# Kernel tuning notes

Hardware: AMD Instinct MI355X
Metric: run time of the kernel (lower is better)

Reference implementation:

```python
import jax, jax.numpy as jnp
from jax import lax
import numpy as np

NEG_SLOPE = 0.01  # torch leaky_relu default
KSIZE = 5

def lrelu(x):
    return jax.nn.leaky_relu(x, NEG_SLOPE)

def conv(x, w, b):
    # x: [N,C,H,W], w: [O,I,kh,kw], valid padding (pad=False in ConvChain)
    y = lax.conv_general_dilated(x, w, (1, 1), 'VALID',
                                 dimension_numbers=('NCHW', 'OIHW', 'NCHW'))
    return y + b[None, :, None, None]

def _forward(features, radiance, global_features,
             emb_w0, emb_b0, emb_w, emb_b,
             pf_w0, pf_b0, pf_w1, pf_b1, pf_w2, pf_b2,
             sf_w, sf_b,
             kp_w0, kp_b0, kp_w1, kp_b1, kp_w2, kp_b2):
    bs, spp, nf, h, w = features.shape
    ngf = global_features.shape[1]
    K = KSIZE

    # --- sample_embedding over all samples at once (replaces per-sp loop) ---
    g = jnp.broadcast_to(global_features, (bs, ngf, h, w))
    x = jnp.concatenate(
        [jnp.broadcast_to(g[:, None], (bs, spp, ngf, h, w)), features], axis=2)
    x = x.reshape(bs * spp, ngf + nf, h, w)
    x = lrelu(conv(x, emb_w0, emb_b0))
    for i in range(5):  # hidden conv layers 1..5
        x = lrelu(conv(x, emb_w[i], emb_b[i]))
    x = conv(x, emb_w[5], emb_b[5])  # linear output layer
    pixel_embed = x.reshape(bs, spp, x.shape[1], x.shape[2], x.shape[3]).max(axis=1)

    # --- pixel_features chain (3 layers, last linear) ---
    p = lrelu(conv(pixel_embed, pf_w0, pf_b0))
    p = lrelu(conv(p, pf_w1, pf_b1))
    pfeat = conv(p, pf_w2, pf_b2)  # [bs, pair_width, ph, pw]
    ph, pw = pfeat.shape[2], pfeat.shape[3]

    # --- crop features/radiance so needed = ph + K - 1 ---
    needed = ph + K - 1
    crop = (h - needed) // 2
    feat_c = features[..., crop:crop + needed, crop:crop + needed]
    rad_c = radiance[..., crop:crop + needed, crop:crop + needed]

    # --- gather K*K taps per pixel (unfold) ---
    taps = jnp.stack([feat_c[..., dy:dy + ph, dx:dx + pw]
                      for dy in range(K) for dx in range(K)], axis=0)
    # [K,K,bs,spp,nf,ph,pw] -> [bs,ph,pw,spp,ky,kx,nf]
    taps = taps.reshape(K, K, bs, spp, nf, ph, pw).transpose(2, 5, 6, 3, 0, 1, 4)
    off = jnp.arange(K, dtype=taps.dtype) - K // 2
    taps = taps.at[..., 0].add(off)            # x += kx - K//2 (kx axis)
    taps = taps.at[..., 1].add(off[:, None])   # y += ky - K//2 (ky axis)

    rt = jnp.stack([rad_c[..., dy:dy + ph, dx:dx + pw]
                    for dy in range(K) for dx in range(K)], axis=0)
    # [K,K,bs,spp,3,ph,pw] -> [bs,3,ph,pw,spp,ky,kx]
    rt = rt.reshape(K, K, bs, spp, 3, ph, pw).transpose(2, 4, 5, 6, 3, 0, 1)

    # --- sample_features: single linear layer (FullyConnected depth=1) ---
    sf = jnp.einsum('...f,of->...o', taps, sf_w) + sf_b  # [b,ph,pw,spp,ky,kx,pair]

    # --- kernel_predictor on pixel_features + sample_features ---
    pairf = pfeat.transpose(0, 2, 3, 1)[:, :, :, None, None, None, :]
    hdd = lrelu(jnp.einsum('...i,oi->...o', pairf + sf, kp_w0) + kp_b0)
    hdd = lrelu(jnp.einsum('...i,oi->...o', hdd, kp_w1) + kp_b1)
    wts = (jnp.einsum('...i,oi->...o', hdd, kp_w2) + kp_b2)[..., 0]  # [b,ph,pw,spp,ky,kx]

    # --- weighted radiance accumulate + normalize ---
    unnorm = jnp.einsum('bhwsyx,bchwsyx->bchw', wts, rt)
    sumw = wts.sum(axis=(3, 4, 5))[:, None]  # [b,1,ph,pw]
    return unnorm / (sumw + 1e-8)


def setup_inputs() -> dict:
    key = jax.random.key(0)
    ks = jax.random.split(key, 24)
    BS, SPP, NF, NGF, H, W = 1, 4, 12, 4, 116, 116
    WIDTH, PAIR = 128, 64
    s = 0.05
    inp = {}
    inp['features'] = jax.random.normal(ks[0], (BS, SPP, NF, H, W), jnp.float32)
    inp['radiance'] = jax.random.uniform(ks[1], (BS, SPP, 3, H, W), jnp.float32)
    inp['global_features'] = jax.random.normal(ks[2], (BS, NGF, 1, 1), jnp.float32)
    # sample_embedding: 7 conv layers (first 16->128, rest 128->128, last linear)
    inp['emb_w0'] = jax.random.normal(ks[3], (WIDTH, NF + NGF, 3, 3)) * s
    inp['emb_b0'] = jax.random.normal(ks[4], (WIDTH,)) * s
    inp['emb_w'] = jax.random.normal(ks[5], (6, WIDTH, WIDTH, 3, 3)) * s
    inp['emb_b'] = jax.random.normal(ks[6], (6, WIDTH)) * s
    # pixel_features: 3 conv layers 128->128->128->64 (last linear)
    inp['pf_w0'] = jax.random.normal(ks[7], (WIDTH, WIDTH, 3, 3)) * s
    inp['pf_b0'] = jax.random.normal(ks[8], (WIDTH,)) * s
    inp['pf_w1'] = jax.random.normal(ks[9], (WIDTH, WIDTH, 3, 3)) * s
    inp['pf_b1'] = jax.random.normal(ks[10], (WIDTH,)) * s
    inp['pf_w2'] = jax.random.normal(ks[11], (PAIR, WIDTH, 3, 3)) * s
    inp['pf_b2'] = jax.random.normal(ks[12], (PAIR,)) * s
    # sample_features: FullyConnected(12 -> 64, depth=1) = single linear
    inp['sf_w'] = jax.random.normal(ks[13], (PAIR, NF)) * s
    inp['sf_b'] = jax.random.normal(ks[14], (PAIR,)) * s
    # kernel_predictor: FullyConnected(64 -> 1, depth=3)
    inp['kp_w0'] = jax.random.normal(ks[15], (PAIR, PAIR)) * s
    inp['kp_b0'] = jax.random.normal(ks[16], (PAIR,)) * s
    inp['kp_w1'] = jax.random.normal(ks[17], (PAIR, PAIR)) * s
    inp['kp_b1'] = jax.random.normal(ks[18], (PAIR,)) * s
    inp['kp_w2'] = jax.random.normal(ks[19], (1, PAIR)) * s
    inp['kp_b2'] = jax.random.normal(ks[20], (1,)) * s
    return inp


def reference(features, radiance, global_features,
              emb_w0, emb_b0, emb_w, emb_b,
              pf_w0, pf_b0, pf_w1, pf_b1, pf_w2, pf_b2,
              sf_w, sf_b,
              kp_w0, kp_b0, kp_w1, kp_b1, kp_w2, kp_b2):
    return _forward(features, radiance, global_features,
                    emb_w0, emb_b0, emb_w, emb_b,
                    pf_w0, pf_b0, pf_w1, pf_b1, pf_w2, pf_b2,
                    sf_w, sf_b,
                    kp_w0, kp_b0, kp_w1, kp_b1, kp_w2, kp_b2)
```

## Files before the change

kernel.cpp:

```cpp
#include <hip/hip_runtime.h>


#define HW2 13456
#define NF  12
#define NGF 4

__device__ __forceinline__ float lrelu_f(float x) { return x > 0.f ? x : 0.01f * x; }

__global__ __launch_bounds__(256) void k_buildx0(const float* __restrict__ features,
                                                 const float* __restrict__ gf,
                                                 float* __restrict__ out) {
    int i = blockIdx.x * 256 + threadIdx.x;
    const int total = 4 * 16 * HW2;
    if (i >= total) return;
    int n  = i / (16 * HW2);
    int r  = i - n * (16 * HW2);
    int c  = r / HW2;
    int yx = r - c * HW2;
    float v = (c < NGF) ? gf[c] : features[(n * NF + (c - NGF)) * HW2 + yx];
    out[i] = v;
}

__global__ __launch_bounds__(256) void k_wt(const float* __restrict__ w,
                                            float* __restrict__ wt,
                                            int Cout, int Cin) {
    int i = blockIdx.x * 256 + threadIdx.x;
    int total = Cout * Cin * 9;
    if (i >= total) return;
    int m   = i / (Cin * 9);
    int r   = i - m * (Cin * 9);
    int cin = r / 9;
    int kyx = r - cin * 9;
    wt[(kyx * Cin + cin) * Cout + m] = w[i];
}

__global__ __launch_bounds__(256) void k_wt2(const float* __restrict__ w,
                                             float* __restrict__ wt) {
    int i = blockIdx.x * 256 + threadIdx.x;
    if (i >= 4096) return;
    int o = i >> 6, k = i & 63;
    wt[k * 64 + o] = w[i];
}

template <int CIN, int COUT>
__global__ __launch_bounds__(512) void k_convw(const float* __restrict__ in,
                                               const float* __restrict__ wt,
                                               const float* __restrict__ bias,
                                               float* __restrict__ out,
                                               int H, int W, int relu, int tout) {
    constexpr int MW = COUT / 8;
    const int OH = H - 2, OW = W - 2;
    const int n   = blockIdx.z;
    const int tid = threadIdx.x, lane = tid & 63;
    const int wv  = __builtin_amdgcn_readfirstlane(tid >> 6);
    const int mbase = wv * MW;
    const int lx = lane & 31, lyh = lane >> 5;
    const int oy = blockIdx.y * 2 + lyh;
    const int ox = blockIdx.x * 32 + lx;
    const int cx = min(ox, OW - 1);

    const float* inb = in + (size_t)n * CIN * H * W;
    const int HW = H * W;

    float acc[MW];
    #pragma unroll
    for (int mi = 0; mi < MW; ++mi) acc[mi] = 0.f;

    #pragma unroll
    for (int ky = 0; ky < 3; ++ky) {
        #pragma unroll
        for (int kx = 0; kx < 3; ++kx) {
            const float* ia = inb + (oy + ky) * W + (cx + kx);
            const float* wr = wt + (size_t)((ky * 3 + kx) * CIN) * COUT + mbase;
            #pragma unroll 2
            for (int cin = 0; cin < CIN; ++cin) {
                float v = ia[cin * HW];
                const float* w = wr + cin * COUT;
                #pragma unroll
                for (int mi = 0; mi < MW; ++mi)
                    acc[mi] += w[mi] * v;
            }
        }
    }

    if (ox < OW) {
        if (tout) {
            float* ob = out + (size_t)(oy * OW + ox) * COUT;
            #pragma unroll
            for (int mi = 0; mi < MW; ++mi) {
                int m = mbase + mi;
                float val = acc[mi] + bias[m];
                if (relu) val = lrelu_f(val);
                ob[m] = val;
            }
        } else {
            #pragma unroll
            for (int mi = 0; mi < MW; ++mi) {
                int m = mbase + mi;
                float val = acc[mi] + bias[m];
                if (relu) val = lrelu_f(val);
                out[(((size_t)n * COUT + m) * OH + oy) * OW + ox] = val;
            }
        }
    }
}

__global__ __launch_bounds__(256) void k_sppmax(const float* __restrict__ in,
                                                float* __restrict__ out) {
    int i = blockIdx.x * 256 + threadIdx.x;
    const int total = 128 * 102 * 102;
    if (i >= total) return;
    float m = in[i];
    #pragma unroll
    for (int s = 1; s < 4; ++s) m = fmaxf(m, in[i + s * total]);
    out[i] = m;
}

__global__ __launch_bounds__(256) void k_mlp(const float* __restrict__ features,
                                             const float* __restrict__ pfeat_t,
                                             const float* __restrict__ sf_w,
                                             const float* __restrict__ sf_b,
                                             const float* __restrict__ w0t,
                                             const float* __restrict__ b0,
                                             const float* __restrict__ w1t,
                                             const float* __restrict__ b1,
                                             const float* __restrict__ w2, const float* __restrict__ b2,
                                             float* __restrict__ wts) {
    __shared__ float vx[64][256];
    const int t   = threadIdx.x;
    const int gid = blockIdx.x * 256 + t;
    {
        int p  = gid / 100;
        int r  = gid - p * 100;
        int s  = r / 25;
        int tp = r - s * 25;
        int dy = tp / 5;
        int dx = tp - dy * 5;
        int h  = p / 96;
        int w  = p - h * 96;

        int y = 8 + h + dy, x = 8 + w + dx;
        const float* fb = features + (size_t)(s * NF) * HW2 + (size_t)y * 116 + x;
        float f[12];
        #pragma unroll
        for (int i = 0; i < 12; ++i) f[i] = fb[i * HW2];
        f[0] += (float)(dx - 2);
        f[1] += (float)(dy - 2);

        const float* pft = pfeat_t + (size_t)p * 64;
        #pragma unroll
        for (int o = 0; o < 64; ++o) {
            float a = 0.f;
            #pragma unroll
            for (int i = 0; i < 12; ++i) a += sf_w[o * 12 + i] * f[i];
            a += sf_b[o];
            vx[o][t] = pft[o] + a;
        }
    }
    __syncthreads();

    const int lane = t & 63;
    const int og   = 16 * __builtin_amdgcn_readfirstlane(t >> 6);
    const int tl   = lane * 4;

    {
        float acc[16][4];
        #pragma unroll
        for (int j = 0; j < 16; ++j)
            #pragma unroll
            for (int c = 0; c < 4; ++c) acc[j][c] = 0.f;
        #pragma unroll 4
        for (int k = 0; k < 64; ++k) {
            float4 xv = *(const float4*)(&vx[k][tl]);
            const float* wr = w0t + k * 64 + og;
            #pragma unroll
            for (int j = 0; j < 16; ++j) {
                float wj = wr[j];
                acc[j][0] += wj * xv.x; acc[j][1] += wj * xv.y;
                acc[j][2] += wj * xv.z; acc[j][3] += wj * xv.w;
            }
        }
        __syncthreads();
        #pragma unroll
        for (int j = 0; j < 16; ++j) {
            float bj = b0[og + j];
            float4 ov;
            ov.x = lrelu_f(acc[j][0] + bj); ov.y = lrelu_f(acc[j][1] + bj);
            ov.z = lrelu_f(acc[j][2] + bj); ov.w = lrelu_f(acc[j][3] + bj);
            *(float4*)(&vx[og + j][tl]) = ov;
        }
        __syncthreads();
    }

    {
        float acc[16][4];
        #pragma unroll
        for (int j = 0; j < 16; ++j)
            #pragma unroll
            for (int c = 0; c < 4; ++c) acc[j][c] = 0.f;
        #pragma unroll 4
        for (int k = 0; k < 64; ++k) {
            float4 xv = *(const float4*)(&vx[k][tl]);
            const float* wr = w1t + k * 64 + og;
            #pragma unroll
            for (int j = 0; j < 16; ++j) {
                float wj = wr[j];
                acc[j][0] += wj * xv.x; acc[j][1] += wj * xv.y;
                acc[j][2] += wj * xv.z; acc[j][3] += wj * xv.w;
            }
        }
        __syncthreads();
        #pragma unroll
        for (int j = 0; j < 16; ++j) {
            float bj = b1[og + j];
            float4 ov;
            ov.x = lrelu_f(acc[j][0] + bj); ov.y = lrelu_f(acc[j][1] + bj);
            ov.z = lrelu_f(acc[j][2] + bj); ov.w = lrelu_f(acc[j][3] + bj);
            *(float4*)(&vx[og + j][tl]) = ov;
        }
        __syncthreads();
    }

    {
        float a = 0.f;
        #pragma unroll
        for (int i = 0; i < 64; ++i) a += w2[i] * vx[i][t];
        a += b2[0];
        wts[gid] = a;
    }
}

__global__ __launch_bounds__(256) void k_reduce(const float* __restrict__ wts,
                                                const float* __restrict__ radiance,
                                                float* __restrict__ out) {
    int p = blockIdx.x * 256 + threadIdx.x;
    if (p >= 9216) return;
    int h = p / 96, w = p - h * 96;
    float sw = 0.f, un0 = 0.f, un1 = 0.f, un2 = 0.f;
    const float* wp = wts + (size_t)p * 100;
    for (int s = 0; s < 4; ++s) {
        #pragma unroll
        for (int dy = 0; dy < 5; ++dy) {
            #pragma unroll
            for (int dx = 0; dx < 5; ++dx) {
                float wv = wp[s * 25 + dy * 5 + dx];
                sw += wv;
                int y = 8 + h + dy, x = 8 + w + dx;
                const float* rb = radiance + (size_t)(s * 3) * HW2 + (size_t)y * 116 + x;
                un0 += wv * rb[0 * HW2];
                un1 += wv * rb[1 * HW2];
                un2 += wv * rb[2 * HW2];
            }
        }
    }
    float inv = 1.f / (sw + 1e-8f);
    out[0 * 9216 + p] = un0 * inv;
    out[1 * 9216 + p] = un1 * inv;
    out[2 * 9216 + p] = un2 * inv;
}

extern "C" void kernel_launch(void* const* d_in, const int* in_sizes, int n_in,
                              void* d_out, int out_size, void* d_ws, size_t ws_size,
                              hipStream_t stream) {
    const float* features = (const float*)d_in[0];
    const float* radiance = (const float*)d_in[1];
    const float* gf       = (const float*)d_in[2];
    const float* emb_w0   = (const float*)d_in[3];
    const float* emb_b0   = (const float*)d_in[4];
    const float* emb_w    = (const float*)d_in[5];
    const float* emb_b    = (const float*)d_in[6];
    const float* pf_w0    = (const float*)d_in[7];
    const float* pf_b0    = (const float*)d_in[8];
    const float* pf_w1    = (const float*)d_in[9];
    const float* pf_b1    = (const float*)d_in[10];
    const float* pf_w2    = (const float*)d_in[11];
    const float* pf_b2    = (const float*)d_in[12];
    const float* sf_w     = (const float*)d_in[13];
    const float* sf_b     = (const float*)d_in[14];
    const float* kp_w0    = (const float*)d_in[15];
    const float* kp_b0    = (const float*)d_in[16];
    const float* kp_w1    = (const float*)d_in[17];
    const float* kp_b1    = (const float*)d_in[18];
    const float* kp_w2    = (const float*)d_in[19];
    const float* kp_b2    = (const float*)d_in[20];
    float* out = (float*)d_out;

    float* WT = (float*)d_ws;
    float* wt0  = WT;
    float* wtE0 = WT + 18432;
    float* wtP0 = WT + 18432 + 6 * 147456;
    float* wtP1 = WT + 1050624;
    float* wtP2 = WT + 1198080;
    float* w0t  = WT + 1271808;
    float* w1t  = WT + 1275904;
    float* A = WT + 1280000;
    float* B = A + 6653952;

    auto wtr = [&](const float* w, float* dst, int Cout, int Cin) {
        int total = Cout * Cin * 9;
        k_wt<<<dim3((total + 255) / 256), 256, 0, stream>>>(w, dst, Cout, Cin);
    };
    wtr(emb_w0, wt0, 128, 16);
    for (int i = 0; i < 6; ++i) wtr(emb_w + i * 147456, wtE0 + i * 147456, 128, 128);
    wtr(pf_w0, wtP0, 128, 128);
    wtr(pf_w1, wtP1, 128, 128);
    wtr(pf_w2, wtP2, 64, 128);
    k_wt2<<<dim3(16), 256, 0, stream>>>(kp_w0, w0t);
    k_wt2<<<dim3(16), 256, 0, stream>>>(kp_w1, w1t);

    k_buildx0<<<dim3((4 * 16 * HW2 + 255) / 256), 256, 0, stream>>>(features, gf, A);

    auto gridc = [](int H, int W, int N) {
        int OH = H - 2, OW = W - 2;
        return dim3((OW + 31) / 32, OH / 2, N);
    };

    k_convw<16, 128><<<gridc(116, 116, 4), 512, 0, stream>>>(A, wt0, emb_b0, B, 116, 116, 1, 0);
    k_convw<128,128><<<gridc(114, 114, 4), 512, 0, stream>>>(B, wtE0 + 0*147456, emb_b + 0*128, A, 114, 114, 1, 0);
    k_convw<128,128><<<gridc(112, 112, 4), 512, 0, stream>>>(A, wtE0 + 1*147456, emb_b + 1*128, B, 112, 112, 1, 0);
    k_convw<128,128><<<gridc(110, 110, 4), 512, 0, stream>>>(B, wtE0 + 2*147456, emb_b + 2*128, A, 110, 110, 1, 0);
    k_convw<128,128><<<gridc(108, 108, 4), 512, 0, stream>>>(A, wtE0 + 3*147456, emb_b + 3*128, B, 108, 108, 1, 0);
    k_convw<128,128><<<gridc(106, 106, 4), 512, 0, stream>>>(B, wtE0 + 4*147456, emb_b + 4*128, A, 106, 106, 1, 0);
    k_convw<128,128><<<gridc(104, 104, 4), 512, 0, stream>>>(A, wtE0 + 5*147456, emb_b + 5*128, B, 104, 104, 0, 0);

    k_sppmax<<<dim3(1331712 / 256), 256, 0, stream>>>(B, A);

    k_convw<128,128><<<gridc(102, 102, 1), 512, 0, stream>>>(A, wtP0, pf_b0, B, 102, 102, 1, 0);
    k_convw<128,128><<<gridc(100, 100, 1), 512, 0, stream>>>(B, wtP1, pf_b1, A, 100, 100, 1, 0);
    k_convw<128, 64><<<gridc(98,  98,  1), 512, 0, stream>>>(A, wtP2, pf_b2, B, 98,  98,  0, 1);

    k_mlp<<<dim3(3600), 256, 0, stream>>>(features, B, sf_w, sf_b,
                                          w0t, kp_b0, w1t, kp_b1, kp_w2, kp_b2, A);

    k_reduce<<<dim3(36), 256, 0, stream>>>(A, radiance, out);
}
```

Baseline: 2.329 ms.

## Register-block conv over four output rows and more channels per wave

```diff
diff --git a/kernel.cpp b/kernel.cpp
--- a/kernel.cpp
+++ b/kernel.cpp
@@ -43,63 +43,89 @@
 }
 
 template <int CIN, int COUT>
-__global__ __launch_bounds__(512) void k_convw(const float* __restrict__ in,
+__global__ __launch_bounds__(256) void k_convv(const float* __restrict__ in,
                                                const float* __restrict__ wt,
                                                const float* __restrict__ bias,
                                                float* __restrict__ out,
                                                int H, int W, int relu, int tout) {
-    constexpr int MW = COUT / 8;
+    constexpr int MW = COUT / 4;
     const int OH = H - 2, OW = W - 2;
     const int n   = blockIdx.z;
     const int tid = threadIdx.x, lane = tid & 63;
     const int wv  = __builtin_amdgcn_readfirstlane(tid >> 6);
     const int mbase = wv * MW;
-    const int lx = lane & 31, lyh = lane >> 5;
-    const int oy = blockIdx.y * 2 + lyh;
-    const int ox = blockIdx.x * 32 + lx;
+    const int x0 = blockIdx.x * 64, y0 = blockIdx.y * 4;
+    const int ox = x0 + lane;
     const int cx = min(ox, OW - 1);
+    int cy[4];
+    #pragma unroll
+    for (int j = 0; j < 4; ++j) cy[j] = min(y0 + j, OH - 1);
 
     const float* inb = in + (size_t)n * CIN * H * W;
     const int HW = H * W;
 
-    float acc[MW];
+    float acc[MW][4];
     #pragma unroll
-    for (int mi = 0; mi < MW; ++mi) acc[mi] = 0.f;
+    for (int mi = 0; mi < MW; ++mi)
+        #pragma unroll
+        for (int j = 0; j < 4; ++j) acc[mi][j] = 0.f;
 
     #pragma unroll
     for (int ky = 0; ky < 3; ++ky) {
         #pragma unroll
         for (int kx = 0; kx < 3; ++kx) {
-            const float* ia = inb + (oy + ky) * W + (cx + kx);
+            const float* i0 = inb + (cy[0] + ky) * W + cx + kx;
+            const float* i1 = inb + (cy[1] + ky) * W + cx + kx;
+            const float* i2 = inb + (cy[2] + ky) * W + cx + kx;
+            const float* i3 = inb + (cy[3] + ky) * W + cx + kx;
             const float* wr = wt + (size_t)((ky * 3 + kx) * CIN) * COUT + mbase;
             #pragma unroll 2
             for (int cin = 0; cin < CIN; ++cin) {
-                float v = ia[cin * HW];
+                float v0 = i0[cin * HW];
+                float v1 = i1[cin * HW];
+                float v2 = i2[cin * HW];
+                float v3 = i3[cin * HW];
                 const float* w = wr + cin * COUT;
                 #pragma unroll
-                for (int mi = 0; mi < MW; ++mi)
-                    acc[mi] += w[mi] * v;
+                for (int mi = 0; mi < MW; ++mi) {
+                    float wm = w[mi];
+                    acc[mi][0] += wm * v0;
+                    acc[mi][1] += wm * v1;
+                    acc[mi][2] += wm * v2;
+                    acc[mi][3] += wm * v3;
+                }
             }
         }
     }
 
     if (ox < OW) {
         if (tout) {
-            float* ob = out + (size_t)(oy * OW + ox) * COUT;
+            #pragma unroll
+            for (int j = 0; j < 4; ++j) {
+                int oy = y0 + j;
+                if (oy >= OH) continue;
+                float* ob = out + (size_t)(oy * OW + ox) * COUT;
+                #pragma unroll
+                for (int mi = 0; mi < MW; ++mi) {
+                    int m = mbase + mi;
+                    float val = acc[mi][j] + bias[m];
+                    if (relu) val = lrelu_f(val);
+                    ob[m] = val;
+                }
+            }
+        } else {
             #pragma unroll
             for (int mi = 0; mi < MW; ++mi) {
                 int m = mbase + mi;
-                float val = acc[mi] + bias[m];
-                if (relu) val = lrelu_f(val);
-                ob[m] = val;
-            }
-        } else {
-            #pragma unroll
-            for (int mi = 0; mi < MW; ++mi) {
-                int m = mbase + mi;
-                float val = acc[mi] + bias[m];
-                if (relu) val = lrelu_f(val);
-                out[(((size_t)n * COUT + m) * OH + oy) * OW + ox] = val;
+                float bv = bias[m];
+                #pragma unroll
+                for (int j = 0; j < 4; ++j) {
+                    int oy = y0 + j;
+                    if (oy >= OH) continue;
+                    float val = acc[mi][j] + bv;
+                    if (relu) val = lrelu_f(val);
+                    out[(((size_t)n * COUT + m) * OH + oy) * OW + ox] = val;
+                }
             }
         }
     }
@@ -312,22 +338,22 @@
 
     auto gridc = [](int H, int W, int N) {
         int OH = H - 2, OW = W - 2;
-        return dim3((OW + 31) / 32, OH / 2, N);
+        return dim3((OW + 63) / 64, (OH + 3) / 4, N);
     };
 
-    k_convw<16, 128><<<gridc(116, 116, 4), 512, 0, stream>>>(A, wt0, emb_b0, B, 116, 116, 1, 0);
-    k_convw<128,128><<<gridc(114, 114, 4), 512, 0, stream>>>(B, wtE0 + 0*147456, emb_b + 0*128, A, 114, 114, 1, 0);
-    k_convw<128,128><<<gridc(112, 112, 4), 512, 0, stream>>>(A, wtE0 + 1*147456, emb_b + 1*128, B, 112, 112, 1, 0);
-    k_convw<128,128><<<gridc(110, 110, 4), 512, 0, stream>>>(B, wtE0 + 2*147456, emb_b + 2*128, A, 110, 110, 1, 0);
-    k_convw<128,128><<<gridc(108, 108, 4), 512, 0, stream>>>(A, wtE0 + 3*147456, emb_b + 3*128, B, 108, 108, 1, 0);
-    k_convw<128,128><<<gridc(106, 106, 4), 512, 0, stream>>>(B, wtE0 + 4*147456, emb_b + 4*128, A, 106, 106, 1, 0);
-    k_convw<128,128><<<gridc(104, 104, 4), 512, 0, stream>>>(A, wtE0 + 5*147456, emb_b + 5*128, B, 104, 104, 0, 0);
+    k_convv<16, 128><<<gridc(116, 116, 4), 256, 0, stream>>>(A, wt0, emb_b0, B, 116, 116, 1, 0);
+    k_convv<128,128><<<gridc(114, 114, 4), 256, 0, stream>>>(B, wtE0 + 0*147456, emb_b + 0*128, A, 114, 114, 1, 0);
+    k_convv<128,128><<<gridc(112, 112, 4), 256, 0, stream>>>(A, wtE0 + 1*147456, emb_b + 1*128, B, 112, 112, 1, 0);
+    k_convv<128,128><<<gridc(110, 110, 4), 256, 0, stream>>>(B, wtE0 + 2*147456, emb_b + 2*128, A, 110, 110, 1, 0);
+    k_convv<128,128><<<gridc(108, 108, 4), 256, 0, stream>>>(A, wtE0 + 3*147456, emb_b + 3*128, B, 108, 108, 1, 0);
+    k_convv<128,128><<<gridc(106, 106, 4), 256, 0, stream>>>(B, wtE0 + 4*147456, emb_b + 4*128, A, 106, 106, 1, 0);
+    k_convv<128,128><<<gridc(104, 104, 4), 256, 0, stream>>>(A, wtE0 + 5*147456, emb_b + 5*128, B, 104, 104, 0, 0);
 
     k_sppmax<<<dim3(1331712 / 256), 256, 0, stream>>>(B, A);
 
-    k_convw<128,128><<<gridc(102, 102, 1), 512, 0, stream>>>(A, wtP0, pf_b0, B, 102, 102, 1, 0);
-    k_convw<128,128><<<gridc(100, 100, 1), 512, 0, stream>>>(B, wtP1, pf_b1, A, 100, 100, 1, 0);
-    k_convw<128, 64><<<gridc(98,  98,  1), 512, 0, stream>>>(A, wtP2, pf_b2, B, 98,  98,  0, 1);
+    k_convv<128,128><<<gridc(102, 102, 1), 256, 0, stream>>>(A, wtP0, pf_b0, B, 102, 102, 1, 0);
+    k_convv<128,128><<<gridc(100, 100, 1), 256, 0, stream>>>(B, wtP1, pf_b1, A, 100, 100, 1, 0);
+    k_convv<128, 64><<<gridc(98,  98,  1), 256, 0, stream>>>(A, wtP2, pf_b2, B, 98,  98,  0, 1);
 
     k_mlp<<<dim3(3600), 256, 0, stream>>>(features, B, sf_w, sf_b,
                                           w0t, kp_b0, w1t, kp_b1, kp_w2, kp_b2, A);
```

After: 3.365 ms. +44.5%, slower.
